# Performance work log

Measured on AMD Instinct MI355X. Metric: run time of the kernel, lower is better.

## Reference

```python
import jax, jax.numpy as jnp
import numpy as np

B, N, C = 8, 4096, 512
H, DK, DV = 8, 64, 64


def _xnorm(x, gamma):
    # L2 norm over last dim, keepdim; scale by per-head gamma
    nrm = jnp.sqrt(jnp.sum(x * x, axis=-1, keepdims=True))
    return x * gamma / nrm


def setup_inputs() -> dict:
    key = jax.random.key(0)
    ks = jax.random.split(key, 9)
    inp = {
        "queries": jax.random.normal(ks[0], (B, N, C), dtype=jnp.float32),
        "keys": jax.random.normal(ks[1], (B, N, C), dtype=jnp.float32),
        "values": jax.random.normal(ks[2], (B, N, C), dtype=jnp.float32),
        # Linear weights stored torch-style [out, in]; init.normal_(std=0.001), bias=0
        "Wq": jax.random.normal(ks[3], (H * DK, C), dtype=jnp.float32) * 0.001,
        "bq": jnp.zeros((H * DK,), dtype=jnp.float32),
        "Wk": jax.random.normal(ks[4], (H * DK, C), dtype=jnp.float32) * 0.001,
        "bk": jnp.zeros((H * DK,), dtype=jnp.float32),
        "Wv": jax.random.normal(ks[5], (H * DV, C), dtype=jnp.float32) * 0.001,
        "bv": jnp.zeros((H * DV,), dtype=jnp.float32),
        "Wo": jax.random.normal(ks[6], (C, H * DV), dtype=jnp.float32) * 0.001,
        "bo": jnp.zeros((C,), dtype=jnp.float32),
        "gamma": jax.random.normal(ks[7], (1, H, 1, 1), dtype=jnp.float32),
    }
    return inp


def reference(queries, keys, values, Wq, bq, Wk, bk, Wv, bv, Wo, bo, gamma):
    bs, nq, _ = queries.shape
    nk = keys.shape[1]
    # projections -> [b, h, n, d]
    q = (queries @ Wq.T + bq).reshape(bs, nq, H, DK).transpose(0, 2, 1, 3)
    k = (keys @ Wk.T + bk).reshape(bs, nk, H, DK).transpose(0, 2, 1, 3)
    v = (values @ Wv.T + bv).reshape(bs, nk, H, DV).transpose(0, 2, 1, 3)
    # kv: [b, h, dk, dv]  (small intermediate)
    kv = jnp.einsum('bhnk,bhnv->bhkv', k, v)
    kv_n = _xnorm(kv, gamma)     # norm over dv
    q_n = _xnorm(q, gamma)       # norm over dk
    out = jnp.einsum('bhnk,bhkv->bhnv', q_n, kv_n)  # [b,h,nq,dv]
    out = out.transpose(0, 2, 1, 3).reshape(bs, nq, H * DV)
    return out @ Wo.T + bo
```

## Files before the change

### kernel.cpp

```cpp
#include <hip/hip_runtime.h>


typedef __attribute__((ext_vector_type(4))) float f32x4;
typedef __attribute__((ext_vector_type(8))) short s16x8;
typedef __attribute__((ext_vector_type(4))) unsigned short u16x4;
typedef __attribute__((ext_vector_type(8))) unsigned short u16x8;

#define DEVFN __device__ __forceinline__

DEVFN unsigned short f2b(float f) {
  union { float f; unsigned u; } un; un.f = f;
  unsigned r = un.u + 0x7fffu + ((un.u >> 16) & 1u);
  return (unsigned short)(r >> 16);
}
DEVFN float b2f(unsigned short us) {
  union { unsigned u; float f; } un; un.u = ((unsigned)us) << 16;
  return un.f;
}

DEVFN void gl_lds16(const void* g, void* l) {
  __builtin_amdgcn_global_load_lds(
      (const __attribute__((address_space(1))) unsigned*)g,
      (__attribute__((address_space(3))) unsigned*)l, 16, 0, 0);
}

template <bool AF32, typename CT>
DEVFN void gemm_core(const void* Ain, const unsigned short* Bt,
                     const float* bias, CT* C, bool qnorm, const float* gamma,
                     int bx, int by) {
  constexpr int KK = 512, NN = 512;
  __shared__ __align__(16) char AsLDS[AF32 ? 32768 : 16384];
  __shared__ __align__(16) char BsLDS[16384];
  const int tid = threadIdx.x, lane = tid & 63, wid = tid >> 6;
  const int wm = (wid >> 1) * 64, wn = (wid & 1) * 64;
  const int r = lane & 15, g = lane >> 4;

  const char* Bsrc = (const char*)Bt +
      (long)(by * 128 + wid * 32 + (lane >> 3)) * 1024 +
      (((lane & 7) ^ (lane >> 3)) * 16);
  const char* Asrc_e = nullptr;
  const char* Asrc_o = nullptr;
  if constexpr (AF32) {
    const char* ab = (const char*)Ain +
        (long)(bx * 128 + wid * 32 + (lane >> 4)) * 2048;
    Asrc_e = ab + (((lane & 15) ^ (lane >> 4)) * 16);
    Asrc_o = ab + (((lane & 15) ^ (4 + (lane >> 4))) * 16);
  } else {
    Asrc_e = (const char*)Ain +
        (long)(bx * 128 + wid * 32 + (lane >> 3)) * 1024 +
        (((lane & 7) ^ (lane >> 3)) * 16);
  }

  f32x4 acc[4][4] = {};

#define STAGE(KT)                                                              \
  {                                                                            \
    if constexpr (AF32) {                                                      \
      _Pragma("unroll") for (int q = 0; q < 8; ++q)                            \
          gl_lds16((q & 1 ? Asrc_o : Asrc_e) + q * 8192 + (KT)*256,            \
                   AsLDS + (wid * 8 + q) * 1024);                              \
    } else {                                                                   \
      _Pragma("unroll") for (int q = 0; q < 4; ++q)                            \
          gl_lds16(Asrc_e + q * 8192 + (KT)*128,                               \
                   AsLDS + wid * 4096 + q * 1024);                             \
    }                                                                          \
    _Pragma("unroll") for (int q = 0; q < 4; ++q)                              \
        gl_lds16(Bsrc + q * 8192 + (KT)*128,                                   \
                 BsLDS + wid * 4096 + q * 1024);                               \
  }

#define COMPUTE                                                                \
  {                                                                            \
    _Pragma("unroll") for (int ks = 0; ks < 2; ++ks) {                         \
      s16x8 a[4], b[4];                                                        \
      const int kb = ks * 64 + g * 16;                                         \
      _Pragma("unroll") for (int i = 0; i < 4; ++i) {                          \
        int ar = wm + i * 16 + r;                                              \
        if constexpr (AF32) {                                                  \
          const int kc = ks * 128 + g * 32;                                    \
          f32x4 alo = *reinterpret_cast<const f32x4*>(                         \
              AsLDS + ar * 256 + (kc ^ ((ar & 7) << 4)));                      \
          f32x4 ahi = *reinterpret_cast<const f32x4*>(                         \
              AsLDS + ar * 256 + ((kc + 16) ^ ((ar & 7) << 4)));               \
          s16x8 av;                                                            \
          av[0] = (short)f2b(alo[0]); av[1] = (short)f2b(alo[1]);              \
          av[2] = (short)f2b(alo[2]); av[3] = (short)f2b(alo[3]);              \
          av[4] = (short)f2b(ahi[0]); av[5] = (short)f2b(ahi[1]);              \
          av[6] = (short)f2b(ahi[2]); av[7] = (short)f2b(ahi[3]);              \
          a[i] = av;                                                           \
        } else {                                                               \
          a[i] = *reinterpret_cast<const s16x8*>(                              \
              AsLDS + ar * 128 + (kb ^ ((ar & 7) << 4)));                      \
        }                                                                      \
        int br = wn + i * 16 + r;                                              \
        b[i] = *reinterpret_cast<const s16x8*>(                                \
            BsLDS + br * 128 + (kb ^ ((br & 7) << 4)));                        \
      }                                                                        \
      _Pragma("unroll") for (int i = 0; i < 4; ++i)                            \
          _Pragma("unroll") for (int j = 0; j < 4; ++j) acc[i][j] =            \
          __builtin_amdgcn_mfma_f32_16x16x32_bf16(a[i], b[j], acc[i][j], 0,    \
                                                  0, 0);                       \
    }                                                                          \
  }

#define SYNC __syncthreads();

  STAGE(0) SYNC
  COMPUTE SYNC STAGE(1) SYNC
  COMPUTE SYNC STAGE(2) SYNC
  COMPUTE SYNC STAGE(3) SYNC
  COMPUTE SYNC STAGE(4) SYNC
  COMPUTE SYNC STAGE(5) SYNC
  COMPUTE SYNC STAGE(6) SYNC
  COMPUTE SYNC STAGE(7) SYNC
  COMPUTE

#undef STAGE
#undef COMPUTE
#undef SYNC

  const int crow0 = bx * 128 + wm + g * 4;
  const int ccol0 = by * 128 + wn + r;
#pragma unroll
  for (int j = 0; j < 4; ++j) {
    float bv = bias[ccol0 + j * 16];
#pragma unroll
    for (int i = 0; i < 4; ++i)
#pragma unroll
      for (int ii = 0; ii < 4; ++ii) acc[i][j][ii] += bv;
  }
  if (qnorm) {
    const int h = (by * 128 + wn) >> 6;
    const float gam = gamma[h];
#pragma unroll
    for (int i = 0; i < 4; ++i)
#pragma unroll
      for (int ii = 0; ii < 4; ++ii) {
        float s = 0.f;
#pragma unroll
        for (int j = 0; j < 4; ++j) s += acc[i][j][ii] * acc[i][j][ii];
        s += __shfl_xor(s, 1);
        s += __shfl_xor(s, 2);
        s += __shfl_xor(s, 4);
        s += __shfl_xor(s, 8);
        float sc = gam / sqrtf(s);
#pragma unroll
        for (int j = 0; j < 4; ++j) acc[i][j][ii] *= sc;
      }
  }
#pragma unroll
  for (int i = 0; i < 4; ++i)
#pragma unroll
    for (int j = 0; j < 4; ++j)
#pragma unroll
      for (int ii = 0; ii < 4; ++ii) {
        long row = crow0 + i * 16 + ii;
        int col = ccol0 + j * 16;
        if constexpr (sizeof(CT) == 2)
          C[row * NN + col] = f2b(acc[i][j][ii]);
        else
          C[row * NN + col] = acc[i][j][ii];
      }
}

DEVFN void swz_xy(int bid, int nwg, int& bx, int& by) {
  int s = (bid & 7) * (nwg >> 3) + (bid >> 3);
  bx = s >> 2;
  by = s & 3;
}

__global__ __launch_bounds__(256, 3)
void proj_qkv(const float* __restrict__ Aq, const float* __restrict__ Ak,
              const float* __restrict__ Av, const unsigned short* __restrict__ Bq,
              const unsigned short* __restrict__ Bk, const unsigned short* __restrict__ Bv,
              const float* __restrict__ bq, const float* __restrict__ bk,
              const float* __restrict__ bv, unsigned short* __restrict__ Cq,
              unsigned short* __restrict__ Ck, unsigned short* __restrict__ Cv,
              const float* __restrict__ gamma) {
  const int z = blockIdx.z;
  const float* A = z == 0 ? Aq : (z == 1 ? Ak : Av);
  const unsigned short* B = z == 0 ? Bq : (z == 1 ? Bk : Bv);
  const float* bias = z == 0 ? bq : (z == 1 ? bk : bv);
  unsigned short* C = z == 0 ? Cq : (z == 1 ? Ck : Cv);
  int bx, by;
  swz_xy(blockIdx.x, 1024, bx, by);
  gemm_core<true, unsigned short>(A, B, bias, C, z == 0, gamma, bx, by);
}

__global__ __launch_bounds__(256, 3)
void gemm_final(const unsigned short* __restrict__ q, const unsigned short* __restrict__ Mt,
                const float* __restrict__ bo, float* __restrict__ out) {
  const int zb = blockIdx.z;
  int bx, by;
  swz_xy(blockIdx.x, 128, bx, by);
  gemm_core<false, float>(q + (long)zb * 2097152, Mt + (long)zb * 262144, bo,
                          out + (long)zb * 2097152, false, nullptr, bx, by);
}

#define NCHUNK 16
__global__ __launch_bounds__(256, 2)
void kv_partial(const unsigned short* __restrict__ kq,
                const unsigned short* __restrict__ vq,
                float* __restrict__ part) {
  const int tid = threadIdx.x;
  const int chunk = blockIdx.x;
  const int bh = blockIdx.y;
  const int b = bh >> 3, h = bh & 7;
  __shared__ float ks[32][64];
  __shared__ float vs[32][64];
  const int dk0 = (tid & 15) * 4;
  const int dv0 = (tid >> 4) * 4;
  float acc[4][4] = {};
  const long nbase = (long)b * 4096 + chunk * 256;

  for (int sub = 0; sub < 8; ++sub) {
    long n0 = nbase + sub * 32;
#pragma unroll
    for (int i = 0; i < 2; ++i) {
      int e = i * 256 + tid;
      int row = e >> 4, c4 = e & 15;
      long gofs = (n0 + row) * 512 + h * 64 + c4 * 4;
      u16x4 kk = *reinterpret_cast<const u16x4*>(kq + gofs);
      u16x4 vv = *reinterpret_cast<const u16x4*>(vq + gofs);
      f32x4 kf = {b2f(kk[0]), b2f(kk[1]), b2f(kk[2]), b2f(kk[3])};
      f32x4 vf = {b2f(vv[0]), b2f(vv[1]), b2f(vv[2]), b2f(vv[3])};
      *reinterpret_cast<f32x4*>(&ks[row][c4 * 4]) = kf;
      *reinterpret_cast<f32x4*>(&vs[row][c4 * 4]) = vf;
    }
    __syncthreads();
#pragma unroll 4
    for (int n = 0; n < 32; ++n) {
      f32x4 kk = *reinterpret_cast<const f32x4*>(&ks[n][dk0]);
      f32x4 vv = *reinterpret_cast<const f32x4*>(&vs[n][dv0]);
#pragma unroll
      for (int a = 0; a < 4; ++a)
#pragma unroll
        for (int c = 0; c < 4; ++c)
          acc[a][c] += kk[a] * vv[c];
    }
    __syncthreads();
  }
  float* pg = part + ((long)chunk * 64 + bh) * 4096;
#pragma unroll
  for (int a = 0; a < 4; ++a) {
    f32x4 o = {acc[a][0], acc[a][1], acc[a][2], acc[a][3]};
    *reinterpret_cast<f32x4*>(pg + (dk0 + a) * 64 + dv0) = o;
  }
}

__global__ __launch_bounds__(256)
void kv_normN(const float* __restrict__ part, const float* __restrict__ gamma,
              unsigned short* __restrict__ kvn) {
  const int bh = blockIdx.x, h = bh & 7;
  const int tid = threadIdx.x;
  __shared__ float kvs[4096];
  __shared__ float scale[64];
#pragma unroll
  for (int i = 0; i < 4; ++i) {
    int e4 = i * 256 + tid;
    const float* p = part + (long)bh * 4096 + e4 * 4;
    f32x4 s = {0.f, 0.f, 0.f, 0.f};
#pragma unroll
    for (int c = 0; c < NCHUNK; ++c) {
      f32x4 v = *reinterpret_cast<const f32x4*>(p + (long)c * 64 * 4096);
      s += v;
    }
    *reinterpret_cast<f32x4*>(kvs + e4 * 4) = s;
  }
  __syncthreads();
  if (tid < 64) {
    float s = 0.f;
    for (int dv = 0; dv < 64; ++dv) { float x = kvs[tid * 64 + dv]; s += x * x; }
    scale[tid] = gamma[h] / sqrtf(s);
  }
  __syncthreads();
#pragma unroll
  for (int i = 0; i < 4; ++i) {
    int e4 = i * 256 + tid;
    float sc = scale[e4 >> 4];
    f32x4 v = *reinterpret_cast<const f32x4*>(kvs + e4 * 4);
    u16x4 o = {f2b(v[0] * sc), f2b(v[1] * sc), f2b(v[2] * sc), f2b(v[3] * sc)};
    *reinterpret_cast<u16x4*>(kvn + (long)bh * 4096 + e4 * 4) = o;
  }
}

__global__ __launch_bounds__(64)
void mt_kernel(const unsigned short* __restrict__ Wo_b,
               const unsigned short* __restrict__ kvn,
               unsigned short* __restrict__ Mt) {
  const int bid = blockIdx.x;
  const int bh = bid >> 2, seg = bid & 3;
  const int b = bh >> 3, h = bh & 7;
  const int lane = threadIdx.x;
  const int r = lane & 15, g = lane >> 4;
  f32x4 acc[8][4] = {};
  s16x8 bf[2][4];
#pragma unroll
  for (int ks = 0; ks < 2; ++ks)
#pragma unroll
    for (int j = 0; j < 4; ++j)
      bf[ks][j] = *reinterpret_cast<const s16x8*>(
          kvn + (long)bh * 4096 + (j * 16 + r) * 64 + ks * 32 + g * 8);
#pragma unroll
  for (int ks = 0; ks < 2; ++ks)
#pragma unroll
    for (int i = 0; i < 8; ++i) {
      s16x8 af = *reinterpret_cast<const s16x8*>(
          Wo_b + (long)(seg * 128 + i * 16 + r) * 512 + h * 64 + ks * 32 + g * 8);
#pragma unroll
      for (int j = 0; j < 4; ++j)
        acc[i][j] = __builtin_amdgcn_mfma_f32_16x16x32_bf16(af, bf[ks][j], acc[i][j], 0, 0, 0);
    }
#pragma unroll
  for (int i = 0; i < 8; ++i)
#pragma unroll
    for (int j = 0; j < 4; ++j)
#pragma unroll
      for (int ii = 0; ii < 4; ++ii) {
        int c = seg * 128 + i * 16 + g * 4 + ii;
        int dk = j * 16 + r;
        Mt[(long)b * 262144 + (long)c * 512 + h * 64 + dk] = f2b(acc[i][j][ii]);
      }
}

__global__ void cast4(const float* __restrict__ a0, const float* __restrict__ a1,
                      const float* __restrict__ a2, const float* __restrict__ a3,
                      unsigned short* __restrict__ o0, unsigned short* __restrict__ o1,
                      unsigned short* __restrict__ o2, unsigned short* __restrict__ o3) {
  const int y = blockIdx.y;
  const float* in = y == 0 ? a0 : (y == 1 ? a1 : (y == 2 ? a2 : a3));
  unsigned short* out = y == 0 ? o0 : (y == 1 ? o1 : (y == 2 ? o2 : o3));
  int i = blockIdx.x * 256 + threadIdx.x;
  f32x4 v = reinterpret_cast<const f32x4*>(in)[i];
  reinterpret_cast<u16x4*>(out)[i] = u16x4{f2b(v[0]), f2b(v[1]), f2b(v[2]), f2b(v[3])};
}

extern "C" void kernel_launch(void* const* d_in, const int* in_sizes, int n_in,
                              void* d_out, int out_size, void* d_ws, size_t ws_size,
                              hipStream_t stream) {
  const float* queries = (const float*)d_in[0];
  const float* keys    = (const float*)d_in[1];
  const float* values  = (const float*)d_in[2];
  const float* Wq = (const float*)d_in[3];
  const float* bq = (const float*)d_in[4];
  const float* Wk = (const float*)d_in[5];
  const float* bk = (const float*)d_in[6];
  const float* Wv = (const float*)d_in[7];
  const float* bv = (const float*)d_in[8];
  const float* Wo = (const float*)d_in[9];
  const float* bo = (const float*)d_in[10];
  const float* gamma = (const float*)d_in[11];

  unsigned short* Wq_b = (unsigned short*)d_ws;
  unsigned short* Wk_b = Wq_b + 262144;
  unsigned short* Wv_b = Wk_b + 262144;
  unsigned short* Wo_b = Wv_b + 262144;
  unsigned short* q_b  = Wo_b + 262144;
  unsigned short* kvn  = q_b + 16777216;
  float* part = (float*)(kvn + 262144);
  unsigned short* Mt = (unsigned short*)part;
  unsigned short* k_b = (unsigned short*)d_out;
  unsigned short* v_b = k_b + 16777216;
  float* out = (float*)d_out;

  cast4<<<dim3(256, 4), 256, 0, stream>>>(Wq, Wk, Wv, Wo, Wq_b, Wk_b, Wv_b, Wo_b);

  proj_qkv<<<dim3(1024, 1, 3), 256, 0, stream>>>(
      queries, keys, values, Wq_b, Wk_b, Wv_b, bq, bk, bv, q_b, k_b, v_b, gamma);

  kv_partial<<<dim3(NCHUNK, 64), 256, 0, stream>>>(k_b, v_b, part);
  kv_normN<<<64, 256, 0, stream>>>(part, gamma, kvn);
  mt_kernel<<<256, 64, 0, stream>>>(Wo_b, kvn, Mt);

  gemm_final<<<dim3(128, 1, 8), 256, 0, stream>>>(q_b, Mt, bo, out);
}
```

Before: 192.8 us.

## Double-buffer GEMM K-loop and convert fp32 A to bf16 once before LDS

```diff
diff --git a/kernel.cpp b/kernel.cpp
--- a/kernel.cpp
+++ b/kernel.cpp
@@ -4,7 +4,7 @@
 typedef __attribute__((ext_vector_type(4))) float f32x4;
 typedef __attribute__((ext_vector_type(8))) short s16x8;
 typedef __attribute__((ext_vector_type(4))) unsigned short u16x4;
-typedef __attribute__((ext_vector_type(8))) unsigned short u16x8;
+typedef __attribute__((ext_vector_type(2))) unsigned u32x2;
 
 #define DEVFN __device__ __forceinline__
 
@@ -17,6 +17,11 @@
   union { unsigned u; float f; } un; un.u = ((unsigned)us) << 16;
   return un.f;
 }
+DEVFN unsigned pk2(float x0, float x1) {
+  union { float f; unsigned u; } a, b;
+  a.f = x0; b.f = x1;
+  return __builtin_amdgcn_perm(b.u + 0x8000u, a.u + 0x8000u, 0x07060302u);
+}
 
 DEVFN void gl_lds16(const void* g, void* l) {
   __builtin_amdgcn_global_load_lds(
@@ -28,96 +33,120 @@
 DEVFN void gemm_core(const void* Ain, const unsigned short* Bt,
                      const float* bias, CT* C, bool qnorm, const float* gamma,
                      int bx, int by) {
-  constexpr int KK = 512, NN = 512;
-  __shared__ __align__(16) char AsLDS[AF32 ? 32768 : 16384];
-  __shared__ __align__(16) char BsLDS[16384];
+  constexpr int NN = 512;
+  __shared__ __align__(16) char AsL[2][8192];
+  __shared__ __align__(16) char BsL[2][8192];
   const int tid = threadIdx.x, lane = tid & 63, wid = tid >> 6;
   const int wm = (wid >> 1) * 64, wn = (wid & 1) * 64;
   const int r = lane & 15, g = lane >> 4;
 
   const char* Bsrc = (const char*)Bt +
-      (long)(by * 128 + wid * 32 + (lane >> 3)) * 1024 +
-      (((lane & 7) ^ (lane >> 3)) * 16);
-  const char* Asrc_e = nullptr;
-  const char* Asrc_o = nullptr;
+      (long)(by * 128 + wid * 32 + (lane >> 2)) * 1024 +
+      (((lane & 3) ^ ((lane >> 3) & 3)) * 16);
+
+  const char* AsrcR = nullptr;
+  const char* AsrcG = nullptr;
+  int awr[4];
   if constexpr (AF32) {
-    const char* ab = (const char*)Ain +
-        (long)(bx * 128 + wid * 32 + (lane >> 4)) * 2048;
-    Asrc_e = ab + (((lane & 15) ^ (lane >> 4)) * 16);
-    Asrc_o = ab + (((lane & 15) ^ (4 + (lane >> 4))) * 16);
+    AsrcR = (const char*)Ain + (long)(bx * 128 + (tid >> 1)) * 2048 +
+            (tid & 1) * 64;
+    const int row = tid >> 1, rs = (row >> 1) & 3;
+#pragma unroll
+    for (int j = 0; j < 4; ++j) {
+      int p = (tid & 1) * 4 + j;
+      awr[j] = row * 64 + ((((p >> 1) ^ rs) << 4) | ((p & 1) * 8));
+    }
   } else {
-    Asrc_e = (const char*)Ain +
-        (long)(bx * 128 + wid * 32 + (lane >> 3)) * 1024 +
-        (((lane & 7) ^ (lane >> 3)) * 16);
-  }
-
+    AsrcG = (const char*)Ain +
+        (long)(bx * 128 + wid * 32 + (lane >> 2)) * 1024 +
+        (((lane & 3) ^ ((lane >> 3) & 3)) * 16);
+  }
+
+  f32x4 PA[4];
   f32x4 acc[4][4] = {};
 
-#define STAGE(KT)                                                              \
+#define ISSUE_A(KT)                                                            \
   {                                                                            \
-    if constexpr (AF32) {                                                      \
-      _Pragma("unroll") for (int q = 0; q < 8; ++q)                            \
-          gl_lds16((q & 1 ? Asrc_o : Asrc_e) + q * 8192 + (KT)*256,            \
-                   AsLDS + (wid * 8 + q) * 1024);                              \
-    } else {                                                                   \
-      _Pragma("unroll") for (int q = 0; q < 4; ++q)                            \
-          gl_lds16(Asrc_e + q * 8192 + (KT)*128,                               \
-                   AsLDS + wid * 4096 + q * 1024);                             \
+    _Pragma("unroll") for (int j = 0; j < 4; ++j)                              \
+        PA[j] = *reinterpret_cast<const f32x4*>(AsrcR + (KT)*128 + j * 16);    \
+  }
+
+#define PACK_WRITE_A(BUF)                                                      \
+  {                                                                            \
+    _Pragma("unroll") for (int j = 0; j < 4; ++j) {                            \
+      u32x2 w;                                                                 \
+      w[0] = pk2(PA[j][0], PA[j][1]);                                          \
+      w[1] = pk2(PA[j][2], PA[j][3]);                                          \
+      *reinterpret_cast<u32x2*>(AsL[BUF] + awr[j]) = w;                        \
     }                                                                          \
-    _Pragma("unroll") for (int q = 0; q < 4; ++q)                              \
-        gl_lds16(Bsrc + q * 8192 + (KT)*128,                                   \
-                 BsLDS + wid * 4096 + q * 1024);                               \
-  }
-
-#define COMPUTE                                                                \
+  }
+
+#define STAGE_B(BUF, KT)                                                       \
   {                                                                            \
-    _Pragma("unroll") for (int ks = 0; ks < 2; ++ks) {                         \
-      s16x8 a[4], b[4];                                                        \
-      const int kb = ks * 64 + g * 16;                                         \
-      _Pragma("unroll") for (int i = 0; i < 4; ++i) {                          \
-        int ar = wm + i * 16 + r;                                              \
-        if constexpr (AF32) {                                                  \
-          const int kc = ks * 128 + g * 32;                                    \
-          f32x4 alo = *reinterpret_cast<const f32x4*>(                         \
-              AsLDS + ar * 256 + (kc ^ ((ar & 7) << 4)));                      \
-          f32x4 ahi = *reinterpret_cast<const f32x4*>(                         \
-              AsLDS + ar * 256 + ((kc + 16) ^ ((ar & 7) << 4)));               \
-          s16x8 av;                                                            \
-          av[0] = (short)f2b(alo[0]); av[1] = (short)f2b(alo[1]);              \
-          av[2] = (short)f2b(alo[2]); av[3] = (short)f2b(alo[3]);              \
-          av[4] = (short)f2b(ahi[0]); av[5] = (short)f2b(ahi[1]);              \
-          av[6] = (short)f2b(ahi[2]); av[7] = (short)f2b(ahi[3]);              \
-          a[i] = av;                                                           \
-        } else {                                                               \
-          a[i] = *reinterpret_cast<const s16x8*>(                              \
-              AsLDS + ar * 128 + (kb ^ ((ar & 7) << 4)));                      \
-        }                                                                      \
-        int br = wn + i * 16 + r;                                              \
-        b[i] = *reinterpret_cast<const s16x8*>(                                \
-            BsLDS + br * 128 + (kb ^ ((br & 7) << 4)));                        \
-      }                                                                        \
-      _Pragma("unroll") for (int i = 0; i < 4; ++i)                            \
-          _Pragma("unroll") for (int j = 0; j < 4; ++j) acc[i][j] =            \
-          __builtin_amdgcn_mfma_f32_16x16x32_bf16(a[i], b[j], acc[i][j], 0,    \
-                                                  0, 0);                       \
+    _Pragma("unroll") for (int q = 0; q < 2; ++q)                              \
+        gl_lds16(Bsrc + q * 16384 + (KT)*64,                                   \
+                 BsL[BUF] + (wid * 2 + q) * 1024);                             \
+  }
+
+#define STAGE_AG(BUF, KT)                                                      \
+  {                                                                            \
+    _Pragma("unroll") for (int q = 0; q < 2; ++q)                              \
+        gl_lds16(AsrcG + q * 16384 + (KT)*64,                                  \
+                 AsL[BUF] + (wid * 2 + q) * 1024);                             \
+  }
+
+#define COMPUTE(BUF)                                                           \
+  {                                                                            \
+    s16x8 a[4], b[4];                                                          \
+    _Pragma("unroll") for (int i = 0; i < 4; ++i) {                            \
+      int ar = wm + i * 16 + r;                                                \
+      a[i] = *reinterpret_cast<const s16x8*>(                                  \
+          AsL[BUF] + ar * 64 + ((g ^ ((ar >> 1) & 3)) << 4));                  \
+      int br = wn + i * 16 + r;                                                \
+      b[i] = *reinterpret_cast<const s16x8*>(                                  \
+          BsL[BUF] + br * 64 + ((g ^ ((br >> 1) & 3)) << 4));                  \
     }                                                                          \
-  }
-
-#define SYNC __syncthreads();
-
-  STAGE(0) SYNC
-  COMPUTE SYNC STAGE(1) SYNC
-  COMPUTE SYNC STAGE(2) SYNC
-  COMPUTE SYNC STAGE(3) SYNC
-  COMPUTE SYNC STAGE(4) SYNC
-  COMPUTE SYNC STAGE(5) SYNC
-  COMPUTE SYNC STAGE(6) SYNC
-  COMPUTE SYNC STAGE(7) SYNC
-  COMPUTE
-
-#undef STAGE
+    _Pragma("unroll") for (int i = 0; i < 4; ++i)                              \
+        _Pragma("unroll") for (int j = 0; j < 4; ++j) acc[i][j] =              \
+        __builtin_amdgcn_mfma_f32_16x16x32_bf16(a[i], b[j], acc[i][j], 0, 0,   \
+                                                0);                            \
+  }
+
+#define STEP(CUR, NXT, KT)                                                     \
+  if constexpr (AF32) { ISSUE_A(KT) }                                          \
+  STAGE_B(NXT, KT)                                                             \
+  if constexpr (!AF32) { STAGE_AG(NXT, KT) }                                   \
+  COMPUTE(CUR)                                                                 \
+  if constexpr (AF32) { PACK_WRITE_A(NXT) }                                    \
+  __syncthreads();
+
+  if constexpr (AF32) { ISSUE_A(0) PACK_WRITE_A(0) } else { STAGE_AG(0, 0) }
+  STAGE_B(0, 0)
+  __syncthreads();
+
+  STEP(0, 1, 1)
+  STEP(1, 0, 2)
+  STEP(0, 1, 3)
+  STEP(1, 0, 4)
+  STEP(0, 1, 5)
+  STEP(1, 0, 6)
+  STEP(0, 1, 7)
+  STEP(1, 0, 8)
+  STEP(0, 1, 9)
+  STEP(1, 0, 10)
+  STEP(0, 1, 11)
+  STEP(1, 0, 12)
+  STEP(0, 1, 13)
+  STEP(1, 0, 14)
+  STEP(0, 1, 15)
+  COMPUTE(1)
+
+#undef ISSUE_A
+#undef PACK_WRITE_A
+#undef STAGE_B
+#undef STAGE_AG
 #undef COMPUTE
-#undef SYNC
+#undef STEP
 
   const int crow0 = bx * 128 + wm + g * 4;
   const int ccol0 = by * 128 + wn + r;
```

Result: slower. 204.2 us (+5.9%).

## Rewrite GEMM core as 256x256 tile with double-buffered LDS pipeline

Applied to the files above, without the earlier changes.

```diff
diff --git a/kernel.cpp b/kernel.cpp
--- a/kernel.cpp
+++ b/kernel.cpp
@@ -4,7 +4,7 @@
 typedef __attribute__((ext_vector_type(4))) float f32x4;
 typedef __attribute__((ext_vector_type(8))) short s16x8;
 typedef __attribute__((ext_vector_type(4))) unsigned short u16x4;
-typedef __attribute__((ext_vector_type(8))) unsigned short u16x8;
+typedef __attribute__((ext_vector_type(4))) unsigned u32x4;
 
 #define DEVFN __device__ __forceinline__
 
@@ -17,7 +17,11 @@
   union { unsigned u; float f; } un; un.u = ((unsigned)us) << 16;
   return un.f;
 }
-
+DEVFN unsigned pk2(float x0, float x1) {
+  union { float f; unsigned u; } a, b;
+  a.f = x0; b.f = x1;
+  return __builtin_amdgcn_perm(b.u + 0x8000u, a.u + 0x8000u, 0x07060302u);
+}
 DEVFN void gl_lds16(const void* g, void* l) {
   __builtin_amdgcn_global_load_lds(
       (const __attribute__((address_space(1))) unsigned*)g,
@@ -25,151 +29,250 @@
 }
 
 template <bool AF32, typename CT>
-DEVFN void gemm_core(const void* Ain, const unsigned short* Bt,
-                     const float* bias, CT* C, bool qnorm, const float* gamma,
-                     int bx, int by) {
-  constexpr int KK = 512, NN = 512;
-  __shared__ __align__(16) char AsLDS[AF32 ? 32768 : 16384];
-  __shared__ __align__(16) char BsLDS[16384];
+DEVFN void gemm256(const void* Ain, const unsigned short* Bt,
+                   const float* bias, CT* C, bool qnorm, const float* gamma,
+                   int bx, int by) {
+  constexpr int NN = 512;
+  __shared__ __align__(16) char LA[65536];
+  __shared__ __align__(16) char LB[65536];
   const int tid = threadIdx.x, lane = tid & 63, wid = tid >> 6;
-  const int wm = (wid >> 1) * 64, wn = (wid & 1) * 64;
   const int r = lane & 15, g = lane >> 4;
-
-  const char* Bsrc = (const char*)Bt +
-      (long)(by * 128 + wid * 32 + (lane >> 3)) * 1024 +
-      (((lane & 7) ^ (lane >> 3)) * 16);
-  const char* Asrc_e = nullptr;
-  const char* Asrc_o = nullptr;
+  const int mw = wid >> 2;
+  const int nw = wid & 3;
+
+  const char* pa = LA + mw * 16384 + r * 128;
+  const char* pb = LB + (nw >> 1) * 16384 + ((nw & 1) * 64 + r) * 128;
+  const int sw0 = (g ^ (r & 7)) << 4;
+  const int sw1 = ((4 + g) ^ (r & 7)) << 4;
+
+  const char* BsS = (const char*)Bt + (long)(by * 256 + (tid >> 3)) * 1024 +
+                    ((tid & 7) ^ ((tid >> 3) & 7)) * 16;
+  char* BdS = LB + wid * 1024;
+
+  const char* AsS = nullptr;
+  const char* AfS = nullptr;
+  char* AdS = LA + wid * 1024;
+  int aw0 = 0, aw1 = 0;
   if constexpr (AF32) {
-    const char* ab = (const char*)Ain +
-        (long)(bx * 128 + wid * 32 + (lane >> 4)) * 2048;
-    Asrc_e = ab + (((lane & 15) ^ (lane >> 4)) * 16);
-    Asrc_o = ab + (((lane & 15) ^ (4 + (lane >> 4))) * 16);
+    AfS = (const char*)Ain + (long)(bx * 256 + (tid >> 2)) * 2048 +
+          (tid & 3) * 64;
+    const int rr = tid >> 2, s0 = (tid & 3) * 2;
+    aw0 = rr * 128 + ((s0 ^ (rr & 7)) << 4);
+    aw1 = rr * 128 + (((s0 + 1) ^ (rr & 7)) << 4);
   } else {
-    Asrc_e = (const char*)Ain +
-        (long)(bx * 128 + wid * 32 + (lane >> 3)) * 1024 +
-        (((lane & 7) ^ (lane >> 3)) * 16);
-  }
-
-  f32x4 acc[4][4] = {};
-
-#define STAGE(KT)                                                              \
+    AsS = (const char*)Ain + (long)(bx * 256 + (tid >> 3)) * 1024 +
+          ((tid & 7) ^ ((tid >> 3) & 7)) * 16;
+  }
+
+  f32x4 acc[8][4] = {};
+  s16x8 b0[4], b1[4];
+  f32x4 rs0[4], rs1[4];
+
+#define SB0 __builtin_amdgcn_sched_barrier(0);
+#define BARR SB0 __builtin_amdgcn_s_barrier(); SB0
+#define VMC(N) asm volatile("s_waitcnt vmcnt(" #N ")" ::: "memory");
+#define LGK asm volatile("s_waitcnt lgkmcnt(0)" ::: "memory");
+
+#define RA(dv, BUF, FOFF, SW)                                                  \
+  _Pragma("unroll") for (int f = 0; f < 4; ++f)                                \
+      dv[f] = *reinterpret_cast<const s16x8*>(pa + (BUF)*32768 + (FOFF) +      \
+                                              f * 2048 + (SW));
+#define RB(dv, BUF, SW)                                                        \
+  _Pragma("unroll") for (int j = 0; j < 4; ++j)                                \
+      dv[j] = *reinterpret_cast<const s16x8*>(pb + (BUF)*32768 + j * 2048 +    \
+                                              (SW));
+#define MM(av, bv, FB)                                                         \
+  _Pragma("unroll") for (int f = 0; f < 4; ++f)                                \
+      _Pragma("unroll") for (int j = 0; j < 4; ++j)                            \
+      acc[(FB) + f][j] = __builtin_amdgcn_mfma_f32_16x16x32_bf16(              \
+          av[f], bv[j], acc[(FB) + f][j], 0, 0, 0);
+
+#define SGB(BUF, HALF, KT)                                                     \
+  gl_lds16(BsS + ((HALF)*128) * 1024 + (KT)*128,                               \
+           BdS + (BUF)*32768 + (HALF)*16384);                                  \
+  gl_lds16(BsS + ((HALF)*128 + 64) * 1024 + (KT)*128,                          \
+           BdS + (BUF)*32768 + (HALF)*16384 + 8192);
+#define SGA(BUF, HALF, KT)                                                     \
+  gl_lds16(AsS + ((HALF)*128) * 1024 + (KT)*128,                               \
+           AdS + (BUF)*32768 + (HALF)*16384);                                  \
+  gl_lds16(AsS + ((HALF)*128 + 64) * 1024 + (KT)*128,                          \
+           AdS + (BUF)*32768 + (HALF)*16384 + 8192);
+#define LDA(RS, HALF, KT)                                                      \
+  _Pragma("unroll") for (int u = 0; u < 4; ++u)                                \
+      RS[u] = *reinterpret_cast<const f32x4*>(AfS + (long)(HALF)*262144 +      \
+                                              (KT)*256 + u * 16);
+#define WRA(RS, BUF, HALF)                                                     \
   {                                                                            \
-    if constexpr (AF32) {                                                      \
-      _Pragma("unroll") for (int q = 0; q < 8; ++q)                            \
-          gl_lds16((q & 1 ? Asrc_o : Asrc_e) + q * 8192 + (KT)*256,            \
-                   AsLDS + (wid * 8 + q) * 1024);                              \
-    } else {                                                                   \
-      _Pragma("unroll") for (int q = 0; q < 4; ++q)                            \
-          gl_lds16(Asrc_e + q * 8192 + (KT)*128,                               \
-                   AsLDS + wid * 4096 + q * 1024);                             \
+    unsigned w0 = pk2(RS[0][0], RS[0][1]), w1 = pk2(RS[0][2], RS[0][3]);       \
+    unsigned w2 = pk2(RS[1][0], RS[1][1]), w3 = pk2(RS[1][2], RS[1][3]);       \
+    unsigned w4 = pk2(RS[2][0], RS[2][1]), w5 = pk2(RS[2][2], RS[2][3]);       \
+    unsigned w6 = pk2(RS[3][0], RS[3][1]), w7 = pk2(RS[3][2], RS[3][3]);       \
+    *reinterpret_cast<u32x4*>(LA + (BUF)*32768 + (HALF)*16384 + aw0) =         \
+        u32x4{w0, w1, w2, w3};                                                 \
+    *reinterpret_cast<u32x4*>(LA + (BUF)*32768 + (HALF)*16384 + aw1) =         \
+        u32x4{w4, w5, w6, w7};                                                 \
+  }
+
+  if constexpr (AF32) {
+    LDA(rs0, 0, 0) LDA(rs1, 1, 0)
+    WRA(rs0, 0, 0) WRA(rs1, 0, 1)
+    SGB(0, 0, 0) SGB(0, 1, 0) SGB(1, 0, 1) SGB(1, 1, 1)
+    asm volatile("s_waitcnt vmcnt(0) lgkmcnt(0)" ::: "memory");
+    SB0
+    LDA(rs0, 0, 1) LDA(rs1, 1, 1)
+  } else {
+    SGA(0, 0, 0) SGA(0, 1, 0)
+    SGB(0, 0, 0) SGB(0, 1, 0) SGB(1, 0, 1) SGB(1, 1, 1)
+    VMC(0)
+  }
+  BARR
+
+#define ITER(KT0v, LASTv)                                                      \
+  {                                                                    \
+    s16x8 a[4];                                                                \
+    RA(a, 0, 0, sw0) RB(b0, 0, sw0)                                            \
+    if constexpr (AF32) { WRA(rs0, 1, 0) } else { SGA(1, 0, (KT0v) + 1) }      \
+    BARR __builtin_amdgcn_s_setprio(1); MM(a, b0, 0)                           \
+    __builtin_amdgcn_s_setprio(0);                                             \
+    if constexpr (AF32) { LGK }                                                \
+    BARR                                                                       \
+  }                                                                            \
+  {                                                                    \
+    s16x8 a[4];                                                                \
+    RA(a, 0, 0, sw1) RB(b1, 0, sw1)                                            \
+    if constexpr (AF32) { WRA(rs1, 1, 1) } else { SGA(1, 1, (KT0v) + 1) }      \
+    BARR __builtin_amdgcn_s_setprio(1); MM(a, b1, 0)                           \
+    __builtin_amdgcn_s_setprio(0);                                             \
+    if constexpr (AF32) { LGK }                                                \
+    BARR                                                                       \
+  }                                                                            \
+  {                                                                    \
+    s16x8 a[4];                                                                \
+    RA(a, 0, 8192, sw0)                                                        \
+    if (!(LASTv)) {                                                            \
+      SGB(0, 0, (KT0v) + 2) SB0                                                \
+      if constexpr (AF32) { LDA(rs0, 0, (KT0v) + 2) }                          \
     }                                                                          \
-    _Pragma("unroll") for (int q = 0; q < 4; ++q)                              \
-        gl_lds16(Bsrc + q * 8192 + (KT)*128,                                   \
-                 BsLDS + wid * 4096 + q * 1024);                               \
-  }
-
-#define COMPUTE                                                                \
-  {                                                                            \
-    _Pragma("unroll") for (int ks = 0; ks < 2; ++ks) {                         \
-      s16x8 a[4], b[4];                                                        \
-      const int kb = ks * 64 + g * 16;                                         \
-      _Pragma("unroll") for (int i = 0; i < 4; ++i) {                          \
-        int ar = wm + i * 16 + r;                                              \
-        if constexpr (AF32) {                                                  \
-          const int kc = ks * 128 + g * 32;                                    \
-          f32x4 alo = *reinterpret_cast<const f32x4*>(                         \
-              AsLDS + ar * 256 + (kc ^ ((ar & 7) << 4)));                      \
-          f32x4 ahi = *reinterpret_cast<const f32x4*>(                         \
-              AsLDS + ar * 256 + ((kc + 16) ^ ((ar & 7) << 4)));               \
-          s16x8 av;                                                            \
-          av[0] = (short)f2b(alo[0]); av[1] = (short)f2b(alo[1]);              \
-          av[2] = (short)f2b(alo[2]); av[3] = (short)f2b(alo[3]);              \
-          av[4] = (short)f2b(ahi[0]); av[5] = (short)f2b(ahi[1]);              \
-          av[6] = (short)f2b(ahi[2]); av[7] = (short)f2b(ahi[3]);              \
-          a[i] = av;                                                           \
-        } else {                                                               \
-          a[i] = *reinterpret_cast<const s16x8*>(                              \
-              AsLDS + ar * 128 + (kb ^ ((ar & 7) << 4)));                      \
-        }                                                                      \
-        int br = wn + i * 16 + r;                                              \
-        b[i] = *reinterpret_cast<const s16x8*>(                                \
-            BsLDS + br * 128 + (kb ^ ((br & 7) << 4)));                        \
-      }                                                                        \
-      _Pragma("unroll") for (int i = 0; i < 4; ++i)                            \
-          _Pragma("unroll") for (int j = 0; j < 4; ++j) acc[i][j] =            \
-          __builtin_amdgcn_mfma_f32_16x16x32_bf16(a[i], b[j], acc[i][j], 0,    \
-                                                  0, 0);                       \
+    BARR __builtin_amdgcn_s_setprio(1); MM(a, b0, 4)                           \
+    __builtin_amdgcn_s_setprio(0); BARR                                        \
+  }                                                                            \
+  {                                                                    \
+    s16x8 a[4];                                                                \
+    RA(a, 0, 8192, sw1)                                                        \
+    if (!(LASTv)) {                                                            \
+      SGB(0, 1, (KT0v) + 2) SB0                                                \
+      if constexpr (AF32) { LDA(rs1, 1, (KT0v) + 2) }                          \
+      VMC(4)                                                                   \
+    } else { VMC(0) }                                                          \
+    BARR __builtin_amdgcn_s_setprio(1); MM(a, b1, 4)                           \
+    __builtin_amdgcn_s_setprio(0); BARR                                        \
+  }                                                                            \
+  {                                                                    \
+    s16x8 a[4];                                                                \
+    RA(a, 1, 0, sw0) RB(b0, 1, sw0)                                            \
+    if (!(LASTv)) {                                                            \
+      if constexpr (AF32) { WRA(rs0, 0, 0) } else { SGA(0, 0, (KT0v) + 2) }    \
     }                                                                          \
-  }
-
-#define SYNC __syncthreads();
-
-  STAGE(0) SYNC
-  COMPUTE SYNC STAGE(1) SYNC
-  COMPUTE SYNC STAGE(2) SYNC
-  COMPUTE SYNC STAGE(3) SYNC
-  COMPUTE SYNC STAGE(4) SYNC
-  COMPUTE SYNC STAGE(5) SYNC
-  COMPUTE SYNC STAGE(6) SYNC
-  COMPUTE SYNC STAGE(7) SYNC
-  COMPUTE
-
-#undef STAGE
-#undef COMPUTE
-#undef SYNC
-
-  const int crow0 = bx * 128 + wm + g * 4;
-  const int ccol0 = by * 128 + wn + r;
+    BARR __builtin_amdgcn_s_setprio(1); MM(a, b0, 0)                           \
+    __builtin_amdgcn_s_setprio(0);                                             \
+    if constexpr (AF32) { if (!(LASTv)) { LGK } }                              \
+    BARR                                                                       \
+  }                                                                            \
+  {                                                                    \
+    s16x8 a[4];                                                                \
+    RA(a, 1, 0, sw1) RB(b1, 1, sw1)                                            \
+    if (!(LASTv)) {                                                            \
+      if constexpr (AF32) { WRA(rs1, 0, 1) } else { SGA(0, 1, (KT0v) + 2) }    \
+    }                                                                          \
+    BARR __builtin_amdgcn_s_setprio(1); MM(a, b1, 0)                           \
+    __builtin_amdgcn_s_setprio(0);                                             \
+    if constexpr (AF32) { if (!(LASTv)) { LGK } }                              \
+    BARR                                                                       \
+  }                                                                            \
+  {                                                                    \
+    s16x8 a[4];                                                                \
+    RA(a, 1, 8192, sw0)                                                        \
+    if (!(LASTv)) {                                                            \
+      SGB(1, 0, (KT0v) + 3) SB0                                                \
+      if constexpr (AF32) { LDA(rs0, 0, (KT0v) + 3) }                          \
+    }                                                                          \
+    BARR __builtin_amdgcn_s_setprio(1); MM(a, b0, 4)                           \
+    __builtin_amdgcn_s_setprio(0); BARR                                        \
+  }                                                                            \
+  {                                                                    \
+    s16x8 a[4];                                                                \
+    RA(a, 1, 8192, sw1)                                                        \
+    if (!(LASTv)) {                                                            \
+      SGB(1, 1, (KT0v) + 3) SB0                                                \
+      if constexpr (AF32) { LDA(rs1, 1, (KT0v) + 3) }                          \
+      VMC(4)                                                                   \
+    }                                                                          \
+    BARR __builtin_amdgcn_s_setprio(1); MM(a, b1, 4)                           \
+    __builtin_amdgcn_s_setprio(0); BARR                                        \
+  }
+
+  ITER(0, 0)
+  ITER(2, 0)
+  ITER(4, 0)
+  ITER(6, 1)
+
+#undef ITER
+#undef RA
+#undef RB
+#undef MM
+#undef SGB
+#undef SGA
+#undef LDA
+#undef WRA
+#undef SB0
+#undef BARR
+#undef VMC
+#undef LGK
+
+  const int crow0 = bx * 256 + mw * 128 + g * 4;
+  const int ccol0 = by * 256 + nw * 64 + r;
 #pragma unroll
   for (int j = 0; j < 4; ++j) {
     float bv = bias[ccol0 + j * 16];
 #pragma unroll
-    for (int i = 0; i < 4; ++i)
-#pragma unroll
-      for (int ii = 0; ii < 4; ++ii) acc[i][j][ii] += bv;
+    for (int f = 0; f < 8; ++f)
+#pragma unroll
+      for (int ii = 0; ii < 4; ++ii) acc[f][j][ii] += bv;
   }
   if (qnorm) {
-    const int h = (by * 128 + wn) >> 6;
-    const float gam = gamma[h];
-#pragma unroll
-    for (int i = 0; i < 4; ++i)
+    const float gam = gamma[by * 4 + nw];
+#pragma unroll
+    for (int f = 0; f < 8; ++f)
 #pragma unroll
       for (int ii = 0; ii < 4; ++ii) {
         float s = 0.f;
 #pragma unroll
-        for (int j = 0; j < 4; ++j) s += acc[i][j][ii] * acc[i][j][ii];
+        for (int j = 0; j < 4; ++j) s += acc[f][j][ii] * acc[f][j][ii];
         s += __shfl_xor(s, 1);
         s += __shfl_xor(s, 2);
         s += __shfl_xor(s, 4);
         s += __shfl_xor(s, 8);
         float sc = gam / sqrtf(s);
 #pragma unroll
-        for (int j = 0; j < 4; ++j) acc[i][j][ii] *= sc;
+        for (int j = 0; j < 4; ++j) acc[f][j][ii] *= sc;
       }
   }
 #pragma unroll
-  for (int i = 0; i < 4; ++i)
+  for (int f = 0; f < 8; ++f)
 #pragma unroll
     for (int j = 0; j < 4; ++j)
 #pragma unroll
       for (int ii = 0; ii < 4; ++ii) {
-        long row = crow0 + i * 16 + ii;
+        long row = crow0 + f * 16 + ii;
         int col = ccol0 + j * 16;
         if constexpr (sizeof(CT) == 2)
-          C[row * NN + col] = f2b(acc[i][j][ii]);
+          C[row * NN + col] = f2b(acc[f][j][ii]);
         else
-          C[row * NN + col] = acc[i][j][ii];
+          C[row * NN + col] = acc[f][j][ii];
       }
 }
 
-DEVFN void swz_xy(int bid, int nwg, int& bx, int& by) {
-  int s = (bid & 7) * (nwg >> 3) + (bid >> 3);
-  bx = s >> 2;
-  by = s & 3;
-}
-
-__global__ __launch_bounds__(256, 3)
+__global__ __launch_bounds__(512, 1)
 void proj_qkv(const float* __restrict__ Aq, const float* __restrict__ Ak,
               const float* __restrict__ Av, const unsigned short* __restrict__ Bq,
               const unsigned short* __restrict__ Bk, const unsigned short* __restrict__ Bv,
@@ -177,24 +280,25 @@
               const float* __restrict__ bv, unsigned short* __restrict__ Cq,
               unsigned short* __restrict__ Ck, unsigned short* __restrict__ Cv,
               const float* __restrict__ gamma) {
-  const int z = blockIdx.z;
+  const int z = blockIdx.y;
   const float* A = z == 0 ? Aq : (z == 1 ? Ak : Av);
   const unsigned short* B = z == 0 ? Bq : (z == 1 ? Bk : Bv);
   const float* bias = z == 0 ? bq : (z == 1 ? bk : bv);
   unsigned short* C = z == 0 ? Cq : (z == 1 ? Ck : Cv);
-  int bx, by;
-  swz_xy(blockIdx.x, 1024, bx, by);
-  gemm_core<true, unsigned short>(A, B, bias, C, z == 0, gamma, bx, by);
-}
-
-__global__ __launch_bounds__(256, 3)
+  const int bid = blockIdx.x;
+  const int s = (bid & 7) * 32 + (bid >> 3);
+  gemm256<true, unsigned short>(A, B, bias, C, z == 0, gamma, s >> 1, s & 1);
+}
+
+__global__ __launch_bounds__(512, 1)
 void gemm_final(const unsigned short* __restrict__ q, const unsigned short* __restrict__ Mt,
                 const float* __restrict__ bo, float* __restrict__ out) {
-  const int zb = blockIdx.z;
-  int bx, by;
-  swz_xy(blockIdx.x, 128, bx, by);
-  gemm_core<false, float>(q + (long)zb * 2097152, Mt + (long)zb * 262144, bo,
-                          out + (long)zb * 2097152, false, nullptr, bx, by);
+  const int zb = blockIdx.y;
+  const int bid = blockIdx.x;
+  const int s = (bid & 7) * 4 + (bid >> 3);
+  gemm256<false, float>(q + (long)zb * 2097152, Mt + (long)zb * 262144, bo,
+                        out + (long)zb * 2097152, false, nullptr, s >> 1,
+                        s & 1);
 }
 
 #define NCHUNK 16
@@ -365,12 +469,12 @@
 
   cast4<<<dim3(256, 4), 256, 0, stream>>>(Wq, Wk, Wv, Wo, Wq_b, Wk_b, Wv_b, Wo_b);
 
-  proj_qkv<<<dim3(1024, 1, 3), 256, 0, stream>>>(
+  proj_qkv<<<dim3(256, 3), 512, 0, stream>>>(
       queries, keys, values, Wq_b, Wk_b, Wv_b, bq, bk, bv, q_b, k_b, v_b, gamma);
 
   kv_partial<<<dim3(NCHUNK, 64), 256, 0, stream>>>(k_b, v_b, part);
   kv_normN<<<64, 256, 0, stream>>>(part, gamma, kvn);
   mt_kernel<<<256, 64, 0, stream>>>(Wo_b, kvn, Mt);
 
-  gemm_final<<<dim3(128, 1, 8), 256, 0, stream>>>(q_b, Mt, bo, out);
-}
+  gemm_final<<<dim3(32, 8), 512, 0, stream>>>(q_b, Mt, bo, out);
+}
```

After: 178.5 us. -7.4%, faster.
